# Performance work log

Measured on AMD Instinct MI355X. Metric: run time of the kernel, lower is better.

The kernel has to match this reference:

```python
import jax, jax.numpy as jnp
import numpy as np
from jax import lax

# Dims
HID = 2048          # hidden_size
DI = 4096           # d_inner = expand * hidden
NH = 64             # mamba heads
P = 64              # head dim
N = 128             # d_state
G = 1               # n_groups
K = 4               # conv kernel
IM = 8192           # MLP intermediate
BB, L = 2, 2048
EPS = 1e-5
CONV_DIM = DI + 2 * G * N            # 4352
D_IN_PROJ = 2 * DI + 2 * G * N + NH  # 8512


def rmsnorm(x, w, eps=EPS):
    v = jnp.mean(jnp.square(x), axis=-1, keepdims=True)
    return x * jax.lax.rsqrt(v + eps) * w


def setup_inputs() -> dict:
    key = jax.random.key(0)
    ks = jax.random.split(key, 16)
    s = 0.02
    return {
        "positions": jnp.broadcast_to(jnp.arange(L, dtype=jnp.int32), (BB, L)),
        "hidden_states": jax.random.normal(ks[0], (BB, L, HID), jnp.float32),
        "residual": jax.random.normal(ks[1], (BB, L, HID), jnp.float32),
        "in_proj_w": jax.random.normal(ks[2], (D_IN_PROJ, HID), jnp.float32) * s,
        "conv_w": jax.random.normal(ks[3], (CONV_DIM, K), jnp.float32) * 0.2,
        "conv_b": jax.random.normal(ks[4], (CONV_DIM,), jnp.float32) * 0.02,
        "A_log": jnp.log(jnp.arange(1, NH + 1, dtype=jnp.float32)),
        "D": jnp.ones((NH,), jnp.float32),
        "dt_bias": jax.random.uniform(ks[5], (NH,), jnp.float32, -4.0, -2.0),
        "mixer_norm_w": jnp.ones((DI,), jnp.float32),
        "out_proj_w": jax.random.normal(ks[6], (HID, DI), jnp.float32) * s,
        "input_ln_w": jnp.ones((HID,), jnp.float32),
        "pre_ff_ln_w": jnp.ones((HID,), jnp.float32),
        "gate_up_w": jax.random.normal(ks[7], (2 * IM, HID), jnp.float32) * s,
        "down_w": jax.random.normal(ks[8], (HID, IM), jnp.float32) * s,
    }


def reference(positions, hidden_states, residual, in_proj_w, conv_w, conv_b,
              A_log, D, dt_bias, mixer_norm_w, out_proj_w, input_ln_w,
              pre_ff_ln_w, gate_up_w, down_w):
    del positions  # not used by the mamba mixer math
    B_, Lq, _ = hidden_states.shape

    # --- input RMSNorm with fused residual add ---
    residual = hidden_states + residual
    hs = rmsnorm(residual, input_ln_w)

    # --- Mamba2 mixer ---
    proj = jnp.einsum('bld,ed->ble', hs, in_proj_w)   # [B,L,D_IN_PROJ]
    z = proj[..., :DI]
    xBC = proj[..., DI:DI + CONV_DIM]
    dt = proj[..., DI + CONV_DIM:]                    # [B,L,NH]

    # causal depthwise conv (kernel K) + SiLU
    xp = jnp.pad(xBC, ((0, 0), (K - 1, 0), (0, 0)))
    conv = conv_b
    for k in range(K):
        conv = conv + xp[:, k:k + Lq, :] * conv_w[:, k]
    xBC = jax.nn.silu(conv)

    x = xBC[..., :DI].reshape(B_, Lq, NH, P)
    Bm = xBC[..., DI:DI + G * N].reshape(B_, Lq, G, N)
    Cm = xBC[..., DI + G * N:].reshape(B_, Lq, G, N)
    rep = NH // G
    Bm = jnp.repeat(Bm, rep, axis=2)                  # [B,L,NH,N]
    Cm = jnp.repeat(Cm, rep, axis=2)

    dt = jax.nn.softplus(dt + dt_bias)                # [B,L,NH]
    A = -jnp.exp(A_log)                               # [NH]
    dA = jnp.exp(dt * A)                              # [B,L,NH]

    def step(h, inp):
        x_t, B_t, C_t, dA_t, dt_t = inp               # [B,NH,P],[B,NH,N],[B,NH,N],[B,NH],[B,NH]
        h = dA_t[..., None, None] * h + \
            (dt_t[..., None, None] * x_t[..., None]) * B_t[:, :, None, :]
        y = jnp.einsum('bhpn,bhn->bhp', h, C_t)
        return h, y

    xs = (x.transpose(1, 0, 2, 3), Bm.transpose(1, 0, 2, 3),
          Cm.transpose(1, 0, 2, 3), dA.transpose(1, 0, 2), dt.transpose(1, 0, 2))
    h0 = jnp.zeros((B_, NH, P, N), hidden_states.dtype)
    _, ys = lax.scan(step, h0, xs)                    # [L,B,NH,P]
    y = ys.transpose(1, 0, 2, 3) + D[None, None, :, None] * x
    y = y.reshape(B_, Lq, DI)

    # gated RMSNorm (Mixer2RMSNormGated, n_groups=1)
    y = y * jax.nn.silu(z)
    y = rmsnorm(y, mixer_norm_w)
    mamba_out = jnp.einsum('bld,hd->blh', y, out_proj_w)

    # --- pre-FF RMSNorm with fused residual add ---
    residual2 = mamba_out + residual
    hs2 = rmsnorm(residual2, pre_ff_ln_w)

    # --- gated MLP (SiluAndMul) ---
    gu = jnp.einsum('bld,ed->ble', hs2, gate_up_w)    # [B,L,2*IM]
    act = jax.nn.silu(gu[..., :IM]) * gu[..., IM:]
    out = jnp.einsum('bli,hi->blh', act, down_w)
    return out, residual2
```

## Files before the change

### kernel.cpp

```cpp
#include <hip/hip_runtime.h>

#define T_TOK 4096
#define HID   2048
#define DI    4096
#define NH    64
#define PDIM  64
#define NSTATE 128
#define IM    8192
#define LSEQ  2048
#define CONVD 4352
#define DPROJ 8512
#define DPADR 8704
#define QC    64
#define NCH   32

typedef __bf16 bf16x8 __attribute__((ext_vector_type(8)));
typedef float  f32x4  __attribute__((ext_vector_type(4)));

__device__ __forceinline__ unsigned short f2bf(float f) {
  unsigned u = __float_as_uint(f);
  u = (u + 0x7fffu + ((u >> 16) & 1u)) >> 16;
  return (unsigned short)u;
}
__device__ __forceinline__ float bf2f(unsigned short h) {
  return __uint_as_float(((unsigned)h) << 16);
}
__device__ __forceinline__ float siluf(float x) {
  return x / (1.f + __expf(-x));
}

#define GLL(gaddr, laddr) __builtin_amdgcn_global_load_lds( \
    (const __attribute__((address_space(1))) void*)(gaddr), \
    (__attribute__((address_space(3))) void*)(laddr), 16, 0, 0)

__global__ __launch_bounds__(256) void k_cvt(const float* __restrict__ src,
                                             unsigned short* __restrict__ dst, int n4) {
  int gid = blockIdx.x * 256 + threadIdx.x;
  if (gid >= n4) return;
  float4 v = *(const float4*)&src[(size_t)gid * 4];
  unsigned short* o = dst + (size_t)gid * 4;
  o[0] = f2bf(v.x); o[1] = f2bf(v.y); o[2] = f2bf(v.z); o[3] = f2bf(v.w);
}

__global__ __launch_bounds__(256) void k_cvt_inproj(const float* __restrict__ src,
                                                    unsigned short* __restrict__ dst) {
  int gid = blockIdx.x * 256 + threadIdx.x;
  size_t idx4 = (size_t)gid * 4;
  int r = (int)(idx4 >> 11), k = (int)(idx4 & 2047);
  (void)k;
  unsigned short* o = dst + idx4;
  if (r < DPROJ) {
    float4 v = *(const float4*)&src[(size_t)r * HID + (idx4 & 2047)];
    o[0] = f2bf(v.x); o[1] = f2bf(v.y); o[2] = f2bf(v.z); o[3] = f2bf(v.w);
  } else {
    o[0] = 0; o[1] = 0; o[2] = 0; o[3] = 0;
  }
}

__global__ __launch_bounds__(256) void k_cvt_gu(const float* __restrict__ src,
                                                unsigned short* __restrict__ dst) {
  int gid = blockIdx.x * 256 + threadIdx.x;
  size_t idx4 = (size_t)gid * 4;
  int r = (int)(idx4 >> 11), k = (int)(idx4 & 2047);
  int g = r >> 6, j = r & 63;
  int srcr = (j < 32) ? (g * 32 + j) : (IM + g * 32 + (j - 32));
  float4 v = *(const float4*)&src[(size_t)srcr * HID + k];
  unsigned short* o = dst + idx4;
  o[0] = f2bf(v.x); o[1] = f2bf(v.y); o[2] = f2bf(v.z); o[3] = f2bf(v.w);
}

template <int EPI>
__global__ __launch_bounds__(512, 2)
void gemm8(const unsigned short* __restrict__ A, const unsigned short* __restrict__ W,
           int ntn, int ldo, unsigned short* __restrict__ outp) {
  __shared__ __align__(16) char smem[131072];
  const int t = threadIdx.x;
  const int w = t >> 6, l = t & 63;
  const int lr = l & 15, hi = l >> 4;
  const int wr = w >> 2, wc = w & 3;

  const int q = (int)gridDim.x >> 3;
  const int bid = blockIdx.x;
  const int id2 = (bid & 7) * q + (bid >> 3);
  const int tm = id2 / ntn, tn = id2 % ntn;
  const int m0b = tm << 8, n0b = tn << 8;

  const int srow = t >> 3;
  const int scole = ((t & 7) << 3) ^ ((t & 32) ? 16 : 0);
  const unsigned short* Ag = A + (size_t)(m0b + srow) * 2048 + scole;
  const unsigned short* Wg = W + (size_t)(n0b + srow) * 2048 + scole;
  const int ldsw = w * 1024;

  const int aoff = ((wr * 128 + lr) * 128 + hi * 16) ^ ((lr & 4) ? 32 : 0);
  const int boff = ((wc * 64 + lr) * 128 + hi * 16) ^ ((lr & 4) ? 32 : 0);

#define ISSUE_A(jt, hh, bb) do { int p_ = (hh) * 2;                                   \
    GLL(Ag + (size_t)(p_ * 64) * 2048 + (jt) * 64,                                    \
        smem + (bb) * 65536 + p_ * 8192 + ldsw);                                      \
    GLL(Ag + (size_t)(p_ * 64 + 64) * 2048 + (jt) * 64,                               \
        smem + (bb) * 65536 + p_ * 8192 + 8192 + ldsw); } while (0)
#define ISSUE_B(jt, hh, bb) do { int p_ = (hh) * 2;                                   \
    GLL(Wg + (size_t)(p_ * 64) * 2048 + (jt) * 64,                                    \
        smem + (bb) * 65536 + 32768 + p_ * 8192 + ldsw);                              \
    GLL(Wg + (size_t)(p_ * 64 + 64) * 2048 + (jt) * 64,                               \
        smem + (bb) * 65536 + 32768 + p_ * 8192 + 8192 + ldsw); } while (0)

  f32x4 acc[8][4];
#pragma unroll
  for (int m = 0; m < 8; m++)
#pragma unroll
    for (int n = 0; n < 4; n++) acc[m][n] = (f32x4){0.f, 0.f, 0.f, 0.f};

  ISSUE_A(0, 0, 0); ISSUE_A(0, 1, 0);
  ISSUE_B(0, 0, 0); ISSUE_B(0, 1, 0);
  ISSUE_A(1, 0, 1); ISSUE_A(1, 1, 1);
  asm volatile("s_waitcnt vmcnt(4)" ::: "memory");
  __builtin_amdgcn_s_barrier();

#define CLUSTER(m0_) do {                                                             \
    __builtin_amdgcn_s_setprio(1);                                                    \
    _Pragma("unroll")                                                                 \
    for (int m = m0_; m < m0_ + 2; m++)                                               \
      _Pragma("unroll")                                                               \
      for (int n = 0; n < 4; n++)                                                     \
        _Pragma("unroll")                                                             \
        for (int kk = 0; kk < 2; kk++)                                                \
          acc[m][n] = __builtin_amdgcn_mfma_f32_16x16x32_bf16(afr[m][kk], bfr[n][kk], \
                                                              acc[m][n], 0, 0, 0);    \
    __builtin_amdgcn_s_setprio(0); } while (0)

  for (int j = 0; j < 32; ++j) {
    const int cur = j & 1, nxt = cur ^ 1;
    const char* Ab = smem + cur * 65536;
    const char* Bb = Ab + 32768;
    if (j + 1 < 32) { ISSUE_B(j + 1, 0, nxt); ISSUE_B(j + 1, 1, nxt); }
    bf16x8 bfr[4][2], afr[8][2];
#pragma unroll
    for (int n = 0; n < 4; n++)
#pragma unroll
      for (int kk = 0; kk < 2; kk++)
        bfr[n][kk] = *(const bf16x8*)(Bb + boff + n * 2048 + kk * 64);
#pragma unroll
    for (int m = 0; m < 8; m++)
#pragma unroll
      for (int kk = 0; kk < 2; kk++)
        afr[m][kk] = *(const bf16x8*)(Ab + aoff + m * 2048 + kk * 64);
    __builtin_amdgcn_s_barrier();
    CLUSTER(0);
    __builtin_amdgcn_s_barrier();
    if (j + 2 < 32) ISSUE_A(j + 2, 0, cur);
    CLUSTER(2);
    __builtin_amdgcn_s_barrier();
    if (j + 2 < 32) ISSUE_A(j + 2, 1, cur);
    CLUSTER(4);
    __builtin_amdgcn_s_barrier();
    CLUSTER(6);
    if (j + 2 < 32) { asm volatile("s_waitcnt vmcnt(4)" ::: "memory"); }
    else            { asm volatile("s_waitcnt vmcnt(0)" ::: "memory"); }
    __builtin_amdgcn_s_barrier();
  }

  if constexpr (EPI == 0) {
#pragma unroll
    for (int m = 0; m < 8; m++)
#pragma unroll
      for (int n = 0; n < 4; n++)
#pragma unroll
        for (int r = 0; r < 4; r++) {
          int row = m0b + wr * 128 + m * 16 + hi * 4 + r;
          int col = n0b + wc * 64 + n * 16 + lr;
          outp[(size_t)row * ldo + col] = f2bf(acc[m][n][r]);
        }
  } else {
    const int gbase = (n0b + wc * 64) >> 1;
#pragma unroll
    for (int m = 0; m < 8; m++)
#pragma unroll
      for (int n = 0; n < 2; n++)
#pragma unroll
        for (int r = 0; r < 4; r++) {
          int row = m0b + wr * 128 + m * 16 + hi * 4 + r;
          int col = gbase + n * 16 + lr;
          float g = acc[m][n][r], u = acc[m][n + 2][r];
          outp[(size_t)row * ldo + col] = f2bf(siluf(g) * u);
        }
  }
#undef ISSUE_A
#undef ISSUE_B
#undef CLUSTER
}

template <int EPI>
__global__ __launch_bounds__(256)
void gemm_bt(const unsigned short* __restrict__ A, const unsigned short* __restrict__ W,
             int K, int ldo, void* __restrict__ outp, const float* __restrict__ resid) {
  __shared__ __align__(16) unsigned short As[128 * 64];
  __shared__ __align__(16) unsigned short Ws[128 * 64];
  const int t = threadIdx.x;
  const int w = t >> 6, l = t & 63;
  const int m0 = blockIdx.y << 7;
  const int n0 = blockIdx.x << 7;
  const int lr = l & 15;
  const int lk = (l >> 4) << 3;

  const f32x4 fzero = {0.f, 0.f, 0.f, 0.f};
  f32x4 acc[2][8];
#pragma unroll
  for (int m = 0; m < 2; m++)
#pragma unroll
    for (int n = 0; n < 8; n++) acc[m][n] = fzero;

  const int srow = t >> 3;
  const int scol = (t & 7) << 3;
  const unsigned short* Ag = A + (size_t)(m0 + srow) * K + scol;
  const unsigned short* Wg = W + (size_t)(n0 + srow) * K + scol;
  char* AsB = (char*)As + (size_t)w * 1024;
  char* WsB = (char*)Ws + (size_t)w * 1024;

  const int nkt = K >> 6;
  for (int kt = 0; kt < nkt; ++kt) {
    const int k0 = kt << 6;
#pragma unroll
    for (int i = 0; i < 4; ++i)
      GLL(Ag + (size_t)i * 32 * K + k0, AsB + i * 4096);
#pragma unroll
    for (int i = 0; i < 4; ++i)
      GLL(Wg + (size_t)i * 32 * K + k0, WsB + i * 4096);
    __syncthreads();
#pragma unroll
    for (int kk = 0; kk < 2; ++kk) {
      bf16x8 af[2];
#pragma unroll
      for (int m = 0; m < 2; m++)
        af[m] = *(const bf16x8*)&As[(w * 32 + m * 16 + lr) * 64 + kk * 32 + lk];
#pragma unroll
      for (int n = 0; n < 8; n++) {
        bf16x8 bfr = *(const bf16x8*)&Ws[(n * 16 + lr) * 64 + kk * 32 + lk];
#pragma unroll
        for (int m = 0; m < 2; m++)
          acc[m][n] = __builtin_amdgcn_mfma_f32_16x16x32_bf16(af[m], bfr, acc[m][n], 0, 0, 0);
      }
    }
    __syncthreads();
  }

  const int rbase = (l >> 4) << 2;
#pragma unroll
  for (int m = 0; m < 2; m++)
#pragma unroll
    for (int n = 0; n < 8; n++)
#pragma unroll
      for (int r = 0; r < 4; r++) {
        int row = m0 + w * 32 + m * 16 + rbase + r;
        int col = n0 + n * 16 + lr;
        float v = acc[m][n][r];
        if constexpr (EPI == 1) {
          ((float*)outp)[(size_t)row * ldo + col] = v + resid[(size_t)row * ldo + col];
        } else {
          ((float*)outp)[(size_t)row * ldo + col] = v;
        }
      }
}

__device__ __forceinline__ float block_reduce_sum256(float v, float* sred) {
#pragma unroll
  for (int m = 32; m; m >>= 1) v += __shfl_xor(v, m);
  int t = threadIdx.x;
  if ((t & 63) == 0) sred[t >> 6] = v;
  __syncthreads();
  return sred[0] + sred[1] + sred[2] + sred[3];
}

__global__ __launch_bounds__(256)
void k_addnorm(const float* __restrict__ hin, const float* __restrict__ rin,
               const float* __restrict__ wln, float* __restrict__ rout,
               unsigned short* __restrict__ hbf) {
  __shared__ float sred[4];
  const int tok = blockIdx.x, t = threadIdx.x;
  const size_t base = (size_t)tok * HID + t * 8;
  float4 a0 = *(const float4*)&hin[base];
  float4 a1 = *(const float4*)&hin[base + 4];
  float4 b0 = *(const float4*)&rin[base];
  float4 b1 = *(const float4*)&rin[base + 4];
  float v[8] = {a0.x + b0.x, a0.y + b0.y, a0.z + b0.z, a0.w + b0.w,
                a1.x + b1.x, a1.y + b1.y, a1.z + b1.z, a1.w + b1.w};
  float ss = 0.f;
#pragma unroll
  for (int j = 0; j < 8; j++) ss += v[j] * v[j];
  float tot = block_reduce_sum256(ss, sred);
  float rms = rsqrtf(tot * (1.f / HID) + 1e-5f);
  *(float4*)&rout[base] = (float4){v[0], v[1], v[2], v[3]};
  *(float4*)&rout[base + 4] = (float4){v[4], v[5], v[6], v[7]};
  float4 w0 = *(const float4*)&wln[t * 8];
  float4 w1 = *(const float4*)&wln[t * 8 + 4];
  float wa[8] = {w0.x, w0.y, w0.z, w0.w, w1.x, w1.y, w1.z, w1.w};
  unsigned short o[8];
#pragma unroll
  for (int j = 0; j < 8; j++) o[j] = f2bf(v[j] * rms * wa[j]);
  *(ushort4*)&hbf[base] = *(ushort4*)&o[0];
  *(ushort4*)&hbf[base + 4] = *(ushort4*)&o[4];
}

__global__ __launch_bounds__(256)
void k_rmsnorm_bf(const float* __restrict__ src, const float* __restrict__ wln,
                  unsigned short* __restrict__ dst) {
  __shared__ float sred[4];
  const int tok = blockIdx.x, t = threadIdx.x;
  const size_t base = (size_t)tok * HID + t * 8;
  float4 a0 = *(const float4*)&src[base];
  float4 a1 = *(const float4*)&src[base + 4];
  float v[8] = {a0.x, a0.y, a0.z, a0.w, a1.x, a1.y, a1.z, a1.w};
  float ss = 0.f;
#pragma unroll
  for (int j = 0; j < 8; j++) ss += v[j] * v[j];
  float tot = block_reduce_sum256(ss, sred);
  float rms = rsqrtf(tot * (1.f / HID) + 1e-5f);
  float4 w0 = *(const float4*)&wln[t * 8];
  float4 w1 = *(const float4*)&wln[t * 8 + 4];
  float wa[8] = {w0.x, w0.y, w0.z, w0.w, w1.x, w1.y, w1.z, w1.w};
  unsigned short o[8];
#pragma unroll
  for (int j = 0; j < 8; j++) o[j] = f2bf(v[j] * rms * wa[j]);
  *(ushort4*)&dst[base] = *(ushort4*)&o[0];
  *(ushort4*)&dst[base + 4] = *(ushort4*)&o[4];
}

__global__ __launch_bounds__(256)
void k_gatenorm(const unsigned short* __restrict__ ybuf, const unsigned short* __restrict__ projbf,
                const float* __restrict__ wmix, unsigned short* __restrict__ ynorm) {
  __shared__ float sred[4];
  const int tok = blockIdx.x, t = threadIdx.x;
  const size_t yb = (size_t)tok * DI;
  const size_t pb = (size_t)tok * DPADR;
  float g[16];
  float ss = 0.f;
#pragma unroll
  for (int j = 0; j < 16; j++) {
    int idx = j * 256 + t;
    float yv = bf2f(ybuf[yb + idx]);
    float z = bf2f(projbf[pb + idx]);
    float gg = yv * siluf(z);
    g[j] = gg;
    ss += gg * gg;
  }
  float tot = block_reduce_sum256(ss, sred);
  float rms = rsqrtf(tot * (1.f / DI) + 1e-5f);
#pragma unroll
  for (int j = 0; j < 16; j++) {
    int idx = j * 256 + t;
    ynorm[yb + idx] = f2bf(g[j] * rms * wmix[idx]);
  }
}

__global__ __launch_bounds__(256)
void k_conv(const unsigned short* __restrict__ projbf, const float* __restrict__ cw,
            const float* __restrict__ cb, unsigned short* __restrict__ xbf,
            unsigned short* __restrict__ bcbf) {
  const int c = blockIdx.x * 256 + threadIdx.x;
  const int tk = blockIdx.y;
  const int lpos = tk & (LSEQ - 1);
  float4 wv = *(const float4*)&cw[c * 4];
  float wk[4] = {wv.x, wv.y, wv.z, wv.w};
  float acc = cb[c];
#pragma unroll
  for (int k = 0; k < 4; k++) {
    int lp = lpos - 3 + k;
    if (lp >= 0) acc += bf2f(projbf[(size_t)(tk - 3 + k) * DPADR + DI + c]) * wk[k];
  }
  unsigned short r = f2bf(siluf(acc));
  if (c < DI) xbf[(size_t)tk * DI + c] = r;
  else        bcbf[(size_t)tk * 256 + (c - DI)] = r;
}

__global__ __launch_bounds__(256)
void k_dt(const unsigned short* __restrict__ projbf, const float* __restrict__ dt_bias,
          float* __restrict__ dtg) {
  int gid = blockIdx.x * 256 + threadIdx.x;
  int tk = gid >> 6, hh = gid & 63;
  float x = bf2f(projbf[(size_t)tk * DPADR + (DI + CONVD) + hh]) + dt_bias[hh];
  float dt = (x > 20.f) ? x : log1pf(__expf(x));
  dtg[gid] = dt;
}

__global__ __launch_bounds__(256)
void k_ssd1(const unsigned short* __restrict__ xbf, const unsigned short* __restrict__ bcbf,
            const float* __restrict__ dtg, const float* __restrict__ A_log,
            const float* __restrict__ Dv, unsigned short* __restrict__ ybuf,
            unsigned short* __restrict__ Sc, float* __restrict__ dtsum) {
  __shared__ __align__(16) char smem[60928];
  unsigned short* sBs  = (unsigned short*)(smem);
  unsigned short* sCs  = (unsigned short*)(smem + 16384);
  unsigned short* sMs  = (unsigned short*)(smem + 16384);
  unsigned short* sBsT = (unsigned short*)(smem + 32768);
  unsigned short* sXsT = (unsigned short*)(smem + 51200);
  float* sdt = (float*)(smem + 60416);
  float* sdl = (float*)(smem + 60672);

  const int bi = blockIdx.x;
  const int ch = bi & 31, h = (bi >> 5) & 63, b = bi >> 11;
  const int bh = b * NH + h;
  const int tok0 = b * LSEQ + ch * QC;
  const int t = threadIdx.x;
  const int w = t >> 6, l = t & 63, lr = l & 15, hi = l >> 4;
  const float Ah = -__expf(A_log[h]);
  const float Dh = Dv[h];

  {
    const int srow = t >> 4, scol = (t & 15) * 8;
#pragma unroll
    for (int i = 0; i < 4; i++) {
      const unsigned short* gb = bcbf + (size_t)(tok0 + srow + 16 * i) * 256 + scol;
      GLL(gb, (char*)sBs + i * 4096 + w * 1024);
      GLL(gb + 128, (char*)sCs + i * 4096 + w * 1024);
    }
  }
  if (t < QC) sdt[t] = dtg[(size_t)(tok0 + t) * NH + h];
  __syncthreads();
  if (t < QC) sdl[t] = sdt[t];
  __syncthreads();
  for (int off = 1; off < QC; off <<= 1) {
    float v = 0.f;
    if (t < QC && t >= off) v = sdl[t - off];
    __syncthreads();
    if (t < QC) sdl[t] += v;
    __syncthreads();
  }

  {
    const int s = t >> 2;
    const float DlQ = sdl[QC - 1];
    const float csc = __expf(Ah * (DlQ - sdl[s])) * sdt[s];
    const int n0 = (t & 3) * 32;
#pragma unroll
    for (int j = 0; j < 32; j++) {
      float bv = bf2f(sBs[s * 128 + n0 + j]);
      sBsT[(n0 + j) * 72 + s] = f2bf(csc * bv);
    }
    const int p0 = (t & 3) * 16;
    const unsigned short* gx = xbf + (size_t)(tok0 + s) * DI + h * 64 + p0;
    union { uint4 v; unsigned short u[8]; } x0, x1;
    x0.v = *(const uint4*)gx;
    x1.v = *(const uint4*)(gx + 8);
#pragma unroll
    for (int j = 0; j < 8; j++) {
      sXsT[(p0 + j) * 72 + s] = x0.u[j];
      sXsT[(p0 + 8 + j) * 72 + s] = x1.u[j];
    }
  }
  __syncthreads();

  f32x4 accS[4];
#pragma unroll
  for (int jf = 0; jf < 4; jf++) accS[jf] = (f32x4){0.f, 0.f, 0.f, 0.f};
#pragma unroll
  for (int ks = 0; ks < 4; ks++) {
    bf16x8 a = *(const bf16x8*)&sBs[(w * 16 + lr) * 128 + ks * 32 + hi * 8];
#pragma unroll
    for (int jf = 0; jf < 4; jf++) {
      bf16x8 bb = *(const bf16x8*)&sCs[(jf * 16 + lr) * 128 + ks * 32 + hi * 8];
      accS[jf] = __builtin_amdgcn_mfma_f32_16x16x32_bf16(a, bb, accS[jf], 0, 0, 0);
    }
  }
  __syncthreads();

  {
    const int s0 = w * 16 + hi * 4;
#pragma unroll
    for (int jf = 0; jf < 4; jf++) {
      const int tt = jf * 16 + lr;
      const float dlt = sdl[tt];
      unsigned short mv[4];
#pragma unroll
      for (int r = 0; r < 4; r++) {
        const int ss = s0 + r;
        float val = 0.f;
        if (ss <= tt) val = accS[jf][r] * __expf(Ah * (dlt - sdl[ss])) * sdt[ss];
        mv[r] = f2bf(val);
      }
      *(ushort4*)&sMs[tt * 72 + s0] = *(ushort4*)mv;
    }
  }
  __syncthreads();

  {
    f32x4 accY[4];
#pragma unroll
    for (int jf = 0; jf < 4; jf++) accY[jf] = (f32x4){0.f, 0.f, 0.f, 0.f};
#pragma unroll
    for (int ks = 0; ks < 2; ks++) {
      bf16x8 a = *(const bf16x8*)&sMs[(w * 16 + lr) * 72 + ks * 32 + hi * 8];
#pragma unroll
      for (int jf = 0; jf < 4; jf++) {
        bf16x8 bb = *(const bf16x8*)&sXsT[(jf * 16 + lr) * 72 + ks * 32 + hi * 8];
        accY[jf] = __builtin_amdgcn_mfma_f32_16x16x32_bf16(a, bb, accY[jf], 0, 0, 0);
      }
    }
#pragma unroll
    for (int jf = 0; jf < 4; jf++)
#pragma unroll
      for (int r = 0; r < 4; r++) {
        const int tt = w * 16 + hi * 4 + r;
        const int pp = jf * 16 + lr;
        float xv = bf2f(sXsT[pp * 72 + tt]);
        ybuf[(size_t)(tok0 + tt) * DI + h * 64 + pp] = f2bf(accY[jf][r] + Dh * xv);
      }
  }

  {
    f32x4 accT[8];
#pragma unroll
    for (int jf = 0; jf < 8; jf++) accT[jf] = (f32x4){0.f, 0.f, 0.f, 0.f};
#pragma unroll
    for (int ks = 0; ks < 2; ks++) {
      bf16x8 a = *(const bf16x8*)&sXsT[(w * 16 + lr) * 72 + ks * 32 + hi * 8];
#pragma unroll
      for (int jf = 0; jf < 8; jf++) {
        bf16x8 bb = *(const bf16x8*)&sBsT[(jf * 16 + lr) * 72 + ks * 32 + hi * 8];
        accT[jf] = __builtin_amdgcn_mfma_f32_16x16x32_bf16(a, bb, accT[jf], 0, 0, 0);
      }
    }
    unsigned short* sc = Sc + ((size_t)bh * NCH + ch) * (PDIM * NSTATE);
#pragma unroll
    for (int jf = 0; jf < 8; jf++)
#pragma unroll
      for (int r = 0; r < 4; r++) {
        const int pp = w * 16 + hi * 4 + r;
        const int nn = jf * 16 + lr;
        sc[pp * NSTATE + nn] = f2bf(accT[jf][r]);
      }
  }
  if (t == 0) dtsum[bh * NCH + ch] = sdl[QC - 1];
}

__global__ __launch_bounds__(256)
void k_ssd2(const float* __restrict__ A_log, const float* __restrict__ dtsum,
            unsigned short* __restrict__ ScHt) {
  const int blk = blockIdx.x;
  const int bh = blk >> 3, pg = blk & 7;
  const int t = threadIdx.x;
  const int p = pg * 8 + (t >> 5), n0 = (t & 31) * 4;
  const int h = bh & 63;
  const float Ah = -__expf(A_log[h]);
  float H[4] = {0.f, 0.f, 0.f, 0.f};
  for (int c = 0; c < NCH; c++) {
    size_t base = (((size_t)bh * NCH + c) * PDIM + p) * NSTATE + n0;
    ushort4 sv = *(const ushort4*)&ScHt[base];
    float dec = __expf(Ah * dtsum[bh * NCH + c]);
    ushort4 hv;
    hv.x = f2bf(H[0]); hv.y = f2bf(H[1]); hv.z = f2bf(H[2]); hv.w = f2bf(H[3]);
    *(ushort4*)&ScHt[base] = hv;
    H[0] = dec * H[0] + bf2f(sv.x);
    H[1] = dec * H[1] + bf2f(sv.y);
    H[2] = dec * H[2] + bf2f(sv.z);
    H[3] = dec * H[3] + bf2f(sv.w);
  }
}

__global__ __launch_bounds__(256)
void k_ssd3(const unsigned short* __restrict__ bcbf, const unsigned short* __restrict__ Ht,
            const float* __restrict__ dtg, const float* __restrict__ A_log,
            unsigned short* __restrict__ ybuf) {
  __shared__ __align__(16) char smem[33280];
  unsigned short* sCs = (unsigned short*)(smem);
  unsigned short* sHt = (unsigned short*)(smem + 16384);
  float* sdt = (float*)(smem + 32768);
  float* sdl = (float*)(smem + 33024);

  const int bi = blockIdx.x;
  const int ch = bi & 31, h = (bi >> 5) & 63, b = bi >> 11;
  const int bh = b * NH + h;
  const int tok0 = b * LSEQ + ch * QC;
  const int t = threadIdx.x;
  const int w = t >> 6, l = t & 63, lr = l & 15, hi = l >> 4;
  const float Ah = -__expf(A_log[h]);

  {
    const int srow = t >> 4, scol = (t & 15) * 8;
    const unsigned short* gh = Ht + ((size_t)bh * NCH + ch) * (PDIM * NSTATE);
#pragma unroll
    for (int i = 0; i < 4; i++) {
      const unsigned short* gc = bcbf + (size_t)(tok0 + srow + 16 * i) * 256 + 128 + scol;
      GLL(gc, (char*)sCs + i * 4096 + w * 1024);
      GLL(gh + i * 2048 + t * 8, (char*)sHt + i * 4096 + w * 1024);
    }
  }
  if (t < QC) sdt[t] = dtg[(size_t)(tok0 + t) * NH + h];
  __syncthreads();
  if (t < QC) sdl[t] = sdt[t];
  __syncthreads();
  for (int off = 1; off < QC; off <<= 1) {
    float v = 0.f;
    if (t < QC && t >= off) v = sdl[t - off];
    __syncthreads();
    if (t < QC) sdl[t] += v;
    __syncthreads();
  }

  f32x4 acc[4];
#pragma unroll
  for (int jf = 0; jf < 4; jf++) acc[jf] = (f32x4){0.f, 0.f, 0.f, 0.f};
#pragma unroll
  for (int ks = 0; ks < 4; ks++) {
    bf16x8 a = *(const bf16x8*)&sCs[(w * 16 + lr) * 128 + ks * 32 + hi * 8];
#pragma unroll
    for (int jf = 0; jf < 4; jf++) {
      bf16x8 bb = *(const bf16x8*)&sHt[(jf * 16 + lr) * 128 + ks * 32 + hi * 8];
      acc[jf] = __builtin_amdgcn_mfma_f32_16x16x32_bf16(a, bb, acc[jf], 0, 0, 0);
    }
  }
#pragma unroll
  for (int jf = 0; jf < 4; jf++)
#pragma unroll
    for (int r = 0; r < 4; r++) {
      const int tt = w * 16 + hi * 4 + r;
      const int pp = jf * 16 + lr;
      const float dec = __expf(Ah * sdl[tt]);
      const size_t o = (size_t)(tok0 + tt) * DI + h * 64 + pp;
      ybuf[o] = f2bf(bf2f(ybuf[o]) + dec * acc[jf][r]);
    }
}

static const size_t OFF_WBF_IN  = 0;
static const size_t OFF_WBF_OUT = 35651584;
static const size_t OFF_WBF_GU  = 52428800;
static const size_t OFF_WBF_DN  = 119537664;
static const size_t OFF_RESID   = 153092096;
static const size_t OFF_HSBF    = 186646528;
static const size_t OFF_PROJ    = 203423744;
static const size_t OFF_XBF     = 274726912;
static const size_t OFF_BCBF    = 308281344;
static const size_t OFF_DTG     = 310378496;
static const size_t OFF_YBUF    = 311427072;
static const size_t OFF_SC      = 344981504;
static const size_t OFF_DTSUM   = 412090368;

extern "C" void kernel_launch(void* const* d_in, const int* in_sizes, int n_in,
                              void* d_out, int out_size, void* d_ws, size_t ws_size,
                              hipStream_t stream) {
  (void)in_sizes; (void)n_in; (void)out_size; (void)ws_size;
  const float* hidden   = (const float*)d_in[1];
  const float* resin    = (const float*)d_in[2];
  const float* w_inproj = (const float*)d_in[3];
  const float* conv_w   = (const float*)d_in[4];
  const float* conv_b   = (const float*)d_in[5];
  const float* A_log    = (const float*)d_in[6];
  const float* Dvec     = (const float*)d_in[7];
  const float* dt_bias  = (const float*)d_in[8];
  const float* w_mix    = (const float*)d_in[9];
  const float* w_outp   = (const float*)d_in[10];
  const float* w_ln1    = (const float*)d_in[11];
  const float* w_ln2    = (const float*)d_in[12];
  const float* w_gu     = (const float*)d_in[13];
  const float* w_dn     = (const float*)d_in[14];

  char* ws = (char*)d_ws;
  unsigned short* wbf_in  = (unsigned short*)(ws + OFF_WBF_IN);
  unsigned short* wbf_out = (unsigned short*)(ws + OFF_WBF_OUT);
  unsigned short* wbf_gu  = (unsigned short*)(ws + OFF_WBF_GU);
  unsigned short* wbf_dn  = (unsigned short*)(ws + OFF_WBF_DN);
  float*          residb  = (float*)(ws + OFF_RESID);
  unsigned short* hsbf    = (unsigned short*)(ws + OFF_HSBF);
  unsigned short* projbf  = (unsigned short*)(ws + OFF_PROJ);
  unsigned short* actbf   = (unsigned short*)(ws + OFF_PROJ);
  unsigned short* xbf     = (unsigned short*)(ws + OFF_XBF);
  unsigned short* ynormbf = (unsigned short*)(ws + OFF_XBF);
  unsigned short* bcbf    = (unsigned short*)(ws + OFF_BCBF);
  float*          dtgb    = (float*)(ws + OFF_DTG);
  unsigned short* ybuf    = (unsigned short*)(ws + OFF_YBUF);
  unsigned short* scht    = (unsigned short*)(ws + OFF_SC);
  float*          dtsumb  = (float*)(ws + OFF_DTSUM);

  float* out0 = (float*)d_out;
  float* res2 = out0 + (size_t)T_TOK * HID;

  k_cvt_inproj<<<17408, 256, 0, stream>>>(w_inproj, wbf_in);
  k_cvt<<<8192, 256, 0, stream>>>(w_outp, wbf_out, 2097152);
  k_cvt_gu<<<32768, 256, 0, stream>>>(w_gu, wbf_gu);
  k_cvt<<<16384, 256, 0, stream>>>(w_dn, wbf_dn, 4194304);

  k_addnorm<<<T_TOK, 256, 0, stream>>>(hidden, resin, w_ln1, residb, hsbf);
  gemm8<0><<<34 * 16, 512, 0, stream>>>(hsbf, wbf_in, 34, DPADR, projbf);
  k_conv<<<dim3(17, T_TOK), 256, 0, stream>>>(projbf, conv_w, conv_b, xbf, bcbf);
  k_dt<<<T_TOK * NH / 256, 256, 0, stream>>>(projbf, dt_bias, dtgb);
  k_ssd1<<<4096, 256, 0, stream>>>(xbf, bcbf, dtgb, A_log, Dvec, ybuf, scht, dtsumb);
  k_ssd2<<<1024, 256, 0, stream>>>(A_log, dtsumb, scht);
  k_ssd3<<<4096, 256, 0, stream>>>(bcbf, scht, dtgb, A_log, ybuf);
  k_gatenorm<<<T_TOK, 256, 0, stream>>>(ybuf, projbf, w_mix, ynormbf);
  gemm_bt<1><<<dim3(HID / 128, T_TOK / 128), 256, 0, stream>>>(ynormbf, wbf_out, DI, HID, res2, residb);
  k_rmsnorm_bf<<<T_TOK, 256, 0, stream>>>(res2, w_ln2, hsbf);
  gemm8<2><<<64 * 16, 512, 0, stream>>>(hsbf, wbf_gu, 64, IM, actbf);
  gemm_bt<3><<<dim3(HID / 128, T_TOK / 128), 256, 0, stream>>>(actbf, wbf_dn, IM, HID, out0, nullptr);
}
```

Baseline: 1.167 ms.

## Generalize pipelined 256x256 GEMM over K and use it for out_proj and down_proj

Makes the double-buffered gemm8 kernel take K as a parameter and adds fp32-output epilogues, one with a residual add and one plain. The simple 128x128 gemm_bt kernel is removed, and the out_proj and down_proj GEMMs now run on gemm8. The LDS swizzle gains an extra XOR bit to reduce bank conflicts. The point is better MFMA utilization and prefetch overlap on the two N=2048 GEMMs. The cost is only 128 blocks of 256x256 for those GEMMs, which may leave many CUs idle. The tile mapping now also hardcodes 16 row tiles.

```diff
diff --git a/kernel.cpp b/kernel.cpp
--- a/kernel.cpp
+++ b/kernel.cpp
@@ -46,8 +46,7 @@
                                                     unsigned short* __restrict__ dst) {
   int gid = blockIdx.x * 256 + threadIdx.x;
   size_t idx4 = (size_t)gid * 4;
-  int r = (int)(idx4 >> 11), k = (int)(idx4 & 2047);
-  (void)k;
+  int r = (int)(idx4 >> 11);
   unsigned short* o = dst + idx4;
   if (r < DPROJ) {
     float4 v = *(const float4*)&src[(size_t)r * HID + (idx4 & 2047)];
@@ -72,7 +71,8 @@
 template <int EPI>
 __global__ __launch_bounds__(512, 2)
 void gemm8(const unsigned short* __restrict__ A, const unsigned short* __restrict__ W,
-           int ntn, int ldo, unsigned short* __restrict__ outp) {
+           int K, int ntn, int ldo, void* __restrict__ outp,
+           const float* __restrict__ resid) {
   __shared__ __align__(16) char smem[131072];
   const int t = threadIdx.x;
   const int w = t >> 6, l = t & 63;
@@ -82,27 +82,30 @@
   const int q = (int)gridDim.x >> 3;
   const int bid = blockIdx.x;
   const int id2 = (bid & 7) * q + (bid >> 3);
-  const int tm = id2 / ntn, tn = id2 % ntn;
+  const int tn = id2 >> 4, tm = id2 & 15;
   const int m0b = tm << 8, n0b = tn << 8;
 
   const int srow = t >> 3;
-  const int scole = ((t & 7) << 3) ^ ((t & 32) ? 16 : 0);
-  const unsigned short* Ag = A + (size_t)(m0b + srow) * 2048 + scole;
-  const unsigned short* Wg = W + (size_t)(n0b + srow) * 2048 + scole;
+  const int scole = ((t & 7) << 3) ^ ((t & 32) ? 16 : 0) ^ ((t & 64) ? 32 : 0);
+  const unsigned short* Ag = A + (size_t)(m0b + srow) * K + scole;
+  const unsigned short* Wg = W + (size_t)(n0b + srow) * K + scole;
   const int ldsw = w * 1024;
 
-  const int aoff = ((wr * 128 + lr) * 128 + hi * 16) ^ ((lr & 4) ? 32 : 0);
-  const int boff = ((wc * 64 + lr) * 128 + hi * 16) ^ ((lr & 4) ? 32 : 0);
+  const int fa = ((lr & 4) ? 32 : 0) | ((lr & 8) ? 64 : 0);
+  const int arow = (wr * 128 + lr) * 128 + hi * 16;
+  const int brow = (wc * 64 + lr) * 128 + hi * 16;
+  const int aoffk[2] = {arow ^ fa, (arow + 64) ^ fa};
+  const int boffk[2] = {brow ^ fa, (brow + 64) ^ fa};
 
 #define ISSUE_A(jt, hh, bb) do { int p_ = (hh) * 2;                                   \
-    GLL(Ag + (size_t)(p_ * 64) * 2048 + (jt) * 64,                                    \
+    GLL(Ag + (size_t)(p_ * 64) * K + (jt) * 64,                                       \
         smem + (bb) * 65536 + p_ * 8192 + ldsw);                                      \
-    GLL(Ag + (size_t)(p_ * 64 + 64) * 2048 + (jt) * 64,                               \
+    GLL(Ag + (size_t)(p_ * 64 + 64) * K + (jt) * 64,                                  \
         smem + (bb) * 65536 + p_ * 8192 + 8192 + ldsw); } while (0)
 #define ISSUE_B(jt, hh, bb) do { int p_ = (hh) * 2;                                   \
-    GLL(Wg + (size_t)(p_ * 64) * 2048 + (jt) * 64,                                    \
+    GLL(Wg + (size_t)(p_ * 64) * K + (jt) * 64,                                       \
         smem + (bb) * 65536 + 32768 + p_ * 8192 + ldsw);                              \
-    GLL(Wg + (size_t)(p_ * 64 + 64) * 2048 + (jt) * 64,                               \
+    GLL(Wg + (size_t)(p_ * 64 + 64) * K + (jt) * 64,                                  \
         smem + (bb) * 65536 + 32768 + p_ * 8192 + 8192 + ldsw); } while (0)
 
   f32x4 acc[8][4];
@@ -111,6 +114,7 @@
 #pragma unroll
     for (int n = 0; n < 4; n++) acc[m][n] = (f32x4){0.f, 0.f, 0.f, 0.f};
 
+  const int nkt = K >> 6;
   ISSUE_A(0, 0, 0); ISSUE_A(0, 1, 0);
   ISSUE_B(0, 0, 0); ISSUE_B(0, 1, 0);
   ISSUE_A(1, 0, 1); ISSUE_A(1, 1, 1);
@@ -129,38 +133,39 @@
                                                               acc[m][n], 0, 0, 0);    \
     __builtin_amdgcn_s_setprio(0); } while (0)
 
-  for (int j = 0; j < 32; ++j) {
+  for (int j = 0; j < nkt; ++j) {
     const int cur = j & 1, nxt = cur ^ 1;
     const char* Ab = smem + cur * 65536;
     const char* Bb = Ab + 32768;
-    if (j + 1 < 32) { ISSUE_B(j + 1, 0, nxt); ISSUE_B(j + 1, 1, nxt); }
+    if (j + 1 < nkt) { ISSUE_B(j + 1, 0, nxt); ISSUE_B(j + 1, 1, nxt); }
     bf16x8 bfr[4][2], afr[8][2];
 #pragma unroll
     for (int n = 0; n < 4; n++)
 #pragma unroll
       for (int kk = 0; kk < 2; kk++)
-        bfr[n][kk] = *(const bf16x8*)(Bb + boff + n * 2048 + kk * 64);
+        bfr[n][kk] = *(const bf16x8*)(Bb + boffk[kk] + n * 2048);
 #pragma unroll
     for (int m = 0; m < 8; m++)
 #pragma unroll
       for (int kk = 0; kk < 2; kk++)
-        afr[m][kk] = *(const bf16x8*)(Ab + aoff + m * 2048 + kk * 64);
+        afr[m][kk] = *(const bf16x8*)(Ab + aoffk[kk] + m * 2048);
     __builtin_amdgcn_s_barrier();
     CLUSTER(0);
     __builtin_amdgcn_s_barrier();
-    if (j + 2 < 32) ISSUE_A(j + 2, 0, cur);
+    if (j + 2 < nkt) ISSUE_A(j + 2, 0, cur);
     CLUSTER(2);
     __builtin_amdgcn_s_barrier();
-    if (j + 2 < 32) ISSUE_A(j + 2, 1, cur);
+    if (j + 2 < nkt) ISSUE_A(j + 2, 1, cur);
     CLUSTER(4);
     __builtin_amdgcn_s_barrier();
     CLUSTER(6);
-    if (j + 2 < 32) { asm volatile("s_waitcnt vmcnt(4)" ::: "memory"); }
-    else            { asm volatile("s_waitcnt vmcnt(0)" ::: "memory"); }
+    if (j + 2 < nkt) { asm volatile("s_waitcnt vmcnt(4)" ::: "memory"); }
+    else             { asm volatile("s_waitcnt vmcnt(0)" ::: "memory"); }
     __builtin_amdgcn_s_barrier();
   }
 
   if constexpr (EPI == 0) {
+    unsigned short* op = (unsigned short*)outp;
 #pragma unroll
     for (int m = 0; m < 8; m++)
 #pragma unroll
@@ -169,9 +174,10 @@
         for (int r = 0; r < 4; r++) {
           int row = m0b + wr * 128 + m * 16 + hi * 4 + r;
           int col = n0b + wc * 64 + n * 16 + lr;
-          outp[(size_t)row * ldo + col] = f2bf(acc[m][n][r]);
+          op[(size_t)row * ldo + col] = f2bf(acc[m][n][r]);
         }
-  } else {
+  } else if constexpr (EPI == 2) {
+    unsigned short* op = (unsigned short*)outp;
     const int gbase = (n0b + wc * 64) >> 1;
 #pragma unroll
     for (int m = 0; m < 8; m++)
@@ -182,84 +188,26 @@
           int row = m0b + wr * 128 + m * 16 + hi * 4 + r;
           int col = gbase + n * 16 + lr;
           float g = acc[m][n][r], u = acc[m][n + 2][r];
-          outp[(size_t)row * ldo + col] = f2bf(siluf(g) * u);
+          op[(size_t)row * ldo + col] = f2bf(siluf(g) * u);
+        }
+  } else {
+    float* op = (float*)outp;
+#pragma unroll
+    for (int m = 0; m < 8; m++)
+#pragma unroll
+      for (int n = 0; n < 4; n++)
+#pragma unroll
+        for (int r = 0; r < 4; r++) {
+          int row = m0b + wr * 128 + m * 16 + hi * 4 + r;
+          int col = n0b + wc * 64 + n * 16 + lr;
+          float v = acc[m][n][r];
+          if constexpr (EPI == 1) v += resid[(size_t)row * ldo + col];
+          op[(size_t)row * ldo + col] = v;
         }
   }
 #undef ISSUE_A
 #undef ISSUE_B
 #undef CLUSTER
-}
-
-template <int EPI>
-__global__ __launch_bounds__(256)
-void gemm_bt(const unsigned short* __restrict__ A, const unsigned short* __restrict__ W,
-             int K, int ldo, void* __restrict__ outp, const float* __restrict__ resid) {
-  __shared__ __align__(16) unsigned short As[128 * 64];
-  __shared__ __align__(16) unsigned short Ws[128 * 64];
-  const int t = threadIdx.x;
-  const int w = t >> 6, l = t & 63;
-  const int m0 = blockIdx.y << 7;
-  const int n0 = blockIdx.x << 7;
-  const int lr = l & 15;
-  const int lk = (l >> 4) << 3;
-
-  const f32x4 fzero = {0.f, 0.f, 0.f, 0.f};
-  f32x4 acc[2][8];
-#pragma unroll
-  for (int m = 0; m < 2; m++)
-#pragma unroll
-    for (int n = 0; n < 8; n++) acc[m][n] = fzero;
-
-  const int srow = t >> 3;
-  const int scol = (t & 7) << 3;
-  const unsigned short* Ag = A + (size_t)(m0 + srow) * K + scol;
-  const unsigned short* Wg = W + (size_t)(n0 + srow) * K + scol;
-  char* AsB = (char*)As + (size_t)w * 1024;
-  char* WsB = (char*)Ws + (size_t)w * 1024;
-
-  const int nkt = K >> 6;
-  for (int kt = 0; kt < nkt; ++kt) {
-    const int k0 = kt << 6;
-#pragma unroll
-    for (int i = 0; i < 4; ++i)
-      GLL(Ag + (size_t)i * 32 * K + k0, AsB + i * 4096);
-#pragma unroll
-    for (int i = 0; i < 4; ++i)
-      GLL(Wg + (size_t)i * 32 * K + k0, WsB + i * 4096);
-    __syncthreads();
-#pragma unroll
-    for (int kk = 0; kk < 2; ++kk) {
-      bf16x8 af[2];
-#pragma unroll
-      for (int m = 0; m < 2; m++)
-        af[m] = *(const bf16x8*)&As[(w * 32 + m * 16 + lr) * 64 + kk * 32 + lk];
-#pragma unroll
-      for (int n = 0; n < 8; n++) {
-        bf16x8 bfr = *(const bf16x8*)&Ws[(n * 16 + lr) * 64 + kk * 32 + lk];
-#pragma unroll
-        for (int m = 0; m < 2; m++)
-          acc[m][n] = __builtin_amdgcn_mfma_f32_16x16x32_bf16(af[m], bfr, acc[m][n], 0, 0, 0);
-      }
-    }
-    __syncthreads();
-  }
-
-  const int rbase = (l >> 4) << 2;
-#pragma unroll
-  for (int m = 0; m < 2; m++)
-#pragma unroll
-    for (int n = 0; n < 8; n++)
-#pragma unroll
-      for (int r = 0; r < 4; r++) {
-        int row = m0 + w * 32 + m * 16 + rbase + r;
-        int col = n0 + n * 16 + lr;
-        float v = acc[m][n][r];
-        if constexpr (EPI == 1) {
-          ((float*)outp)[(size_t)row * ldo + col] = v + resid[(size_t)row * ldo + col];
-        } else {
-          ((float*)outp)[(size_t)row * ldo + col] = v;
-        }
-      }
 }
 
 __device__ __forceinline__ float block_reduce_sum256(float v, float* sred) {
@@ -679,15 +627,15 @@
   k_cvt<<<16384, 256, 0, stream>>>(w_dn, wbf_dn, 4194304);
 
   k_addnorm<<<T_TOK, 256, 0, stream>>>(hidden, resin, w_ln1, residb, hsbf);
-  gemm8<0><<<34 * 16, 512, 0, stream>>>(hsbf, wbf_in, 34, DPADR, projbf);
+  gemm8<0><<<34 * 16, 512, 0, stream>>>(hsbf, wbf_in, HID, 34, DPADR, projbf, nullptr);
   k_conv<<<dim3(17, T_TOK), 256, 0, stream>>>(projbf, conv_w, conv_b, xbf, bcbf);
   k_dt<<<T_TOK * NH / 256, 256, 0, stream>>>(projbf, dt_bias, dtgb);
   k_ssd1<<<4096, 256, 0, stream>>>(xbf, bcbf, dtgb, A_log, Dvec, ybuf, scht, dtsumb);
   k_ssd2<<<1024, 256, 0, stream>>>(A_log, dtsumb, scht);
   k_ssd3<<<4096, 256, 0, stream>>>(bcbf, scht, dtgb, A_log, ybuf);
   k_gatenorm<<<T_TOK, 256, 0, stream>>>(ybuf, projbf, w_mix, ynormbf);
-  gemm_bt<1><<<dim3(HID / 128, T_TOK / 128), 256, 0, stream>>>(ynormbf, wbf_out, DI, HID, res2, residb);
+  gemm8<1><<<8 * 16, 512, 0, stream>>>(ynormbf, wbf_out, DI, 8, HID, res2, residb);
   k_rmsnorm_bf<<<T_TOK, 256, 0, stream>>>(res2, w_ln2, hsbf);
-  gemm8<2><<<64 * 16, 512, 0, stream>>>(hsbf, wbf_gu, 64, IM, actbf);
-  gemm_bt<3><<<dim3(HID / 128, T_TOK / 128), 256, 0, stream>>>(actbf, wbf_dn, IM, HID, out0, nullptr);
-}
+  gemm8<2><<<64 * 16, 512, 0, stream>>>(hsbf, wbf_gu, HID, 64, IM, actbf, nullptr);
+  gemm8<3><<<8 * 16, 512, 0, stream>>>(actbf, wbf_dn, IM, 8, HID, out0, nullptr);
+}
```

Result: slower. 1.195 ms (+2.4%).
